# Kernel optimization log

Hardware: AMD Instinct MI355X
Metric: run time of the kernel (lower is better)

Reference implementation:

```python
import jax, jax.numpy as jnp
import numpy as np

B, T, D_F, L = 64, 256, 32, 128

def setup_inputs() -> dict:
    key = jax.random.key(0)
    k1, k2, k3, k4, k5 = jax.random.split(key, 5)
    return {
        "x": jax.random.normal(k1, (B, T, D_F), dtype=jnp.float32),
        "latent": jax.random.normal(k2, (B, T, L), dtype=jnp.float32),
        "kernel": jax.random.normal(k3, (1, 1, D_F, L), dtype=jnp.float32) * (6.0 / (D_F + L)) ** 0.5,
        "bias": jax.random.uniform(k4, (1, 1, D_F, L), dtype=jnp.float32),
        "unnorm_beta": jax.random.uniform(k5, (1, T, 1), dtype=jnp.float32),
    }

def reference(x, latent, kernel, bias, unnorm_beta):
    # features: [B,T,D_f,L]
    features = jax.nn.relu(x[..., None] * kernel + bias)
    # normal equations: X^T X over latent axis -> [B,T,D_f,D_f]
    xtx = jnp.einsum('btdl,btel->btde', features, features)
    xtx_inv = jnp.linalg.inv(xtx)
    # X^T y: [B,T,D_f]
    xty = jnp.einsum('btdl,btl->btd', features, latent)
    scores = jnp.einsum('btde,bte->btd', xtx_inv, xty)  # [B,T,D_f]
    # o_hat: weighted sum of feature rows -> [B,T,L]
    o_hat = jnp.einsum('btd,btdl->btl', scores, features)
    # L1-normalized attention over time: [1,T,1]
    abs_b = jnp.abs(unnorm_beta)
    weights = abs_b / jnp.sum(abs_b, axis=1)
    return jnp.sum(o_hat * weights, axis=1)  # [B,L]
```

## Files before the change

kernel.cpp:

```cpp
#include <hip/hip_runtime.h>
#include <stdint.h>

#define B_ 64
#define T_ 256
#define DF 32
#define L_ 128
#define AW 34
#define SLICE 4352

typedef float  v2f    __attribute__((ext_vector_type(2)));
typedef float  f32x16 __attribute__((ext_vector_type(16)));
typedef short  bf16x8 __attribute__((ext_vector_type(8)));

#define WAVE_SYNC() do { asm volatile("s_waitcnt lgkmcnt(0)" ::: "memory"); \
                         __builtin_amdgcn_sched_barrier(0); } while (0)

template <int IMM>
__device__ __forceinline__ float swz_f(float v) {
    return __builtin_bit_cast(float, __builtin_amdgcn_ds_swizzle(
        __builtin_bit_cast(int, v), IMM));
}
__device__ __forceinline__ uint32_t cvt_pk_bf16(float a, float b) {
    uint32_t r;
    asm("v_cvt_pk_bf16_f32 %0, %1, %2" : "=v"(r) : "v"(a), "v"(b));
    return r;
}
__device__ __forceinline__ float lo_f(uint32_t p) { return __builtin_bit_cast(float, p << 16); }
__device__ __forceinline__ float hi_f(uint32_t p) { return __builtin_bit_cast(float, p & 0xFFFF0000u); }

struct frag3 { bf16x8 h, m, l; };
union U8 { uint32_t u[4]; bf16x8 v; };

__device__ __forceinline__ frag3 split3(float4 a, float4 b) {
    uint32_t h0 = cvt_pk_bf16(a.x, a.y), h1 = cvt_pk_bf16(a.z, a.w);
    uint32_t h2 = cvt_pk_bf16(b.x, b.y), h3 = cvt_pk_bf16(b.z, b.w);
    float e0 = a.x - lo_f(h0), e1 = a.y - hi_f(h0);
    float e2 = a.z - lo_f(h1), e3 = a.w - hi_f(h1);
    float e4 = b.x - lo_f(h2), e5 = b.y - hi_f(h2);
    float e6 = b.z - lo_f(h3), e7 = b.w - hi_f(h3);
    uint32_t m0 = cvt_pk_bf16(e0, e1), m1 = cvt_pk_bf16(e2, e3);
    uint32_t m2 = cvt_pk_bf16(e4, e5), m3 = cvt_pk_bf16(e6, e7);
    float g0 = e0 - lo_f(m0), g1 = e1 - hi_f(m0);
    float g2 = e2 - lo_f(m1), g3 = e3 - hi_f(m1);
    float g4 = e4 - lo_f(m2), g5 = e5 - hi_f(m2);
    float g6 = e6 - lo_f(m3), g7 = e7 - hi_f(m3);
    uint32_t l0 = cvt_pk_bf16(g0, g1), l1 = cvt_pk_bf16(g2, g3);
    uint32_t l2 = cvt_pk_bf16(g4, g5), l3 = cvt_pk_bf16(g6, g7);
    U8 H, M, L;
    H.u[0] = h0; H.u[1] = h1; H.u[2] = h2; H.u[3] = h3;
    M.u[0] = m0; M.u[1] = m1; M.u[2] = m2; M.u[3] = m3;
    L.u[0] = l0; L.u[1] = l1; L.u[2] = l2; L.u[3] = l3;
    frag3 r; r.h = H.v; r.m = M.v; r.l = L.v; return r;
}

__device__ __forceinline__ f32x16 mfma32(bf16x8 a, bf16x8 b, f32x16 c) {
    return __builtin_amdgcn_mfma_f32_32x32x16_bf16(a, b, c, 0, 0, 0);
}

template <int K>
__device__ __forceinline__ void gj_round(float (&A)[33], float& dinv, int r) {
    float piv = swz_f<(K << 5)>(A[K]);
    float ip = __builtin_amdgcn_rcpf(piv);
    ip = ip * (2.0f - piv * ip);
    const bool isk = (r == K);
    float fmul = isk ? 0.f : A[K] * ip;
    dinv = isk ? ip : dinv;
    #pragma unroll
    for (int m = K + 1; m < 33; ++m) {
        float pk = swz_f<(K << 5)>(A[m]);
        A[m] = fmaf(-fmul, pk, A[m]);
    }
}

template <int K>
struct GJ {
    static __device__ __forceinline__ void run(float (&A)[33], float& dinv, int r) {
        gj_round<K>(A, dinv, r);
        GJ<K + 1>::run(A, dinv, r);
    }
};
template <>
struct GJ<32> {
    static __device__ __forceinline__ void run(float (&)[33], float&, int) {}
};

__global__ __launch_bounds__(64) void feat_kernel(
    const float* __restrict__ x,
    const float* __restrict__ latent,
    const float* __restrict__ kern,
    const float* __restrict__ bias,
    const float* __restrict__ beta,
    float* __restrict__ out,
    int mode)
{
    __shared__ __align__(16) char smem[2 * SLICE];
    const int lane = threadIdx.x;
    const int btA  = blockIdx.x * 2;
    const int btB  = btA + 1;

    const int g = lane >> 5;
    const int r = lane & 31;

    float* AsA = reinterpret_cast<float*>(smem);
    float* AsB = reinterpret_cast<float*>(smem + SLICE);

    const float4* kern4 = reinterpret_cast<const float4*>(kern);
    const float4* bias4 = reinterpret_cast<const float4*>(bias);
    const float4* latA4 = reinterpret_cast<const float4*>(latent) + (size_t)btA * 32;
    const float4* latB4 = reinterpret_cast<const float4*>(latent) + (size_t)btB * 32;

    const float xA = x[(size_t)btA * DF + r];
    const float xB = x[(size_t)btB * DF + r];

    f32x16 GA, GB;
    #pragma unroll
    for (int i = 0; i < 16; ++i) { GA[i] = 0.f; GB[i] = 0.f; }
    float ayA = 0.f, ayB = 0.f;

    #pragma unroll 2
    for (int ks = 0; ks < 8; ++ks) {
        const int idx = r * 32 + ks * 4 + g * 2;
        float4 Ka = kern4[idx],  Kb = kern4[idx + 1];
        float4 Ba = bias4[idx],  Bb = bias4[idx + 1];

        float4 faA, fbA, faB, fbB;
        faA.x = fmaxf(fmaf(xA, Ka.x, Ba.x), 0.f);
        faA.y = fmaxf(fmaf(xA, Ka.y, Ba.y), 0.f);
        faA.z = fmaxf(fmaf(xA, Ka.z, Ba.z), 0.f);
        faA.w = fmaxf(fmaf(xA, Ka.w, Ba.w), 0.f);
        fbA.x = fmaxf(fmaf(xA, Kb.x, Bb.x), 0.f);
        fbA.y = fmaxf(fmaf(xA, Kb.y, Bb.y), 0.f);
        fbA.z = fmaxf(fmaf(xA, Kb.z, Bb.z), 0.f);
        fbA.w = fmaxf(fmaf(xA, Kb.w, Bb.w), 0.f);
        faB.x = fmaxf(fmaf(xB, Ka.x, Ba.x), 0.f);
        faB.y = fmaxf(fmaf(xB, Ka.y, Ba.y), 0.f);
        faB.z = fmaxf(fmaf(xB, Ka.z, Ba.z), 0.f);
        faB.w = fmaxf(fmaf(xB, Ka.w, Ba.w), 0.f);
        fbB.x = fmaxf(fmaf(xB, Kb.x, Bb.x), 0.f);
        fbB.y = fmaxf(fmaf(xB, Kb.y, Bb.y), 0.f);
        fbB.z = fmaxf(fmaf(xB, Kb.z, Bb.z), 0.f);
        fbB.w = fmaxf(fmaf(xB, Kb.w, Bb.w), 0.f);

        float4 laA = latA4[ks * 4 + g * 2], lbA = latA4[ks * 4 + g * 2 + 1];
        float4 laB = latB4[ks * 4 + g * 2], lbB = latB4[ks * 4 + g * 2 + 1];
        ayA = fmaf(faA.x, laA.x, ayA); ayA = fmaf(faA.y, laA.y, ayA);
        ayA = fmaf(faA.z, laA.z, ayA); ayA = fmaf(faA.w, laA.w, ayA);
        ayA = fmaf(fbA.x, lbA.x, ayA); ayA = fmaf(fbA.y, lbA.y, ayA);
        ayA = fmaf(fbA.z, lbA.z, ayA); ayA = fmaf(fbA.w, lbA.w, ayA);
        ayB = fmaf(faB.x, laB.x, ayB); ayB = fmaf(faB.y, laB.y, ayB);
        ayB = fmaf(faB.z, laB.z, ayB); ayB = fmaf(faB.w, laB.w, ayB);
        ayB = fmaf(fbB.x, lbB.x, ayB); ayB = fmaf(fbB.y, lbB.y, ayB);
        ayB = fmaf(fbB.z, lbB.z, ayB); ayB = fmaf(fbB.w, lbB.w, ayB);

        frag3 FA = split3(faA, fbA);
        frag3 FB = split3(faB, fbB);
        GA = mfma32(FA.h, FA.h, GA);
        GB = mfma32(FB.h, FB.h, GB);
        GA = mfma32(FA.h, FA.m, GA);
        GB = mfma32(FB.h, FB.m, GB);
        GA = mfma32(FA.m, FA.h, GA);
        GB = mfma32(FB.m, FB.h, GB);
        GA = mfma32(FA.h, FA.l, GA);
        GB = mfma32(FB.h, FB.l, GB);
        GA = mfma32(FA.l, FA.h, GA);
        GB = mfma32(FB.l, FB.h, GB);
        GA = mfma32(FA.m, FA.m, GA);
        GB = mfma32(FB.m, FB.m, GB);
    }
    ayA += __shfl_xor(ayA, 32);
    ayB += __shfl_xor(ayB, 32);

    #pragma unroll
    for (int reg = 0; reg < 16; ++reg) {
        const int row = (reg & 3) + 8 * (reg >> 2) + 4 * g;
        AsA[row * AW + r] = GA[reg];
        AsB[row * AW + r] = GB[reg];
    }
    if (g == 0) AsA[r * AW + 32] = ayA;
    else        AsB[r * AW + 32] = ayB;
    WAVE_SYNC();

    float A[33];
    {
        const float* Amy = g ? AsB : AsA;
        #pragma unroll
        for (int m = 0; m < 16; ++m) {
            v2f t = *reinterpret_cast<const v2f*>(&Amy[r * AW + 2 * m]);
            A[2 * m]     = t[0];
            A[2 * m + 1] = t[1];
        }
        A[32] = Amy[r * AW + 32];
    }

    float dinv = 0.f;
    GJ<0>::run(A, dinv, r);
    const float s = A[32] * dinv;

    {
        float4 oA = make_float4(0.f, 0.f, 0.f, 0.f);
        float4 oB = make_float4(0.f, 0.f, 0.f, 0.f);
        #pragma unroll
        for (int dd = 0; dd < 16; ++dd) {
            int d = g * 16 + dd;
            float4 K  = kern4[d * 32 + r];
            float4 Bv = bias4[d * 32 + r];
            float xvA = __shfl(xA, d);
            float xvB = __shfl(xB, d);
            float sA  = __shfl(s, d);
            float sB  = __shfl(s, 32 + d);
            float fx = fmaxf(fmaf(xvA, K.x, Bv.x), 0.f);
            float fy = fmaxf(fmaf(xvA, K.y, Bv.y), 0.f);
            float fz = fmaxf(fmaf(xvA, K.z, Bv.z), 0.f);
            float fw = fmaxf(fmaf(xvA, K.w, Bv.w), 0.f);
            oA.x = fmaf(sA, fx, oA.x);
            oA.y = fmaf(sA, fy, oA.y);
            oA.z = fmaf(sA, fz, oA.z);
            oA.w = fmaf(sA, fw, oA.w);
            fx = fmaxf(fmaf(xvB, K.x, Bv.x), 0.f);
            fy = fmaxf(fmaf(xvB, K.y, Bv.y), 0.f);
            fz = fmaxf(fmaf(xvB, K.z, Bv.z), 0.f);
            fw = fmaxf(fmaf(xvB, K.w, Bv.w), 0.f);
            oB.x = fmaf(sB, fx, oB.x);
            oB.y = fmaf(sB, fy, oB.y);
            oB.z = fmaf(sB, fz, oB.z);
            oB.w = fmaf(sB, fw, oB.w);
        }
        oA.x += __shfl_xor(oA.x, 32); oA.y += __shfl_xor(oA.y, 32);
        oA.z += __shfl_xor(oA.z, 32); oA.w += __shfl_xor(oA.w, 32);
        oB.x += __shfl_xor(oB.x, 32); oB.y += __shfl_xor(oB.y, 32);
        oB.z += __shfl_xor(oB.z, 32); oB.w += __shfl_xor(oB.w, 32);

        if (mode == 0) {
            if (g == 0) reinterpret_cast<float4*>(out)[(size_t)btA * 32 + r] = oA;
            else        reinterpret_cast<float4*>(out)[(size_t)btB * 32 + r] = oB;
        } else {
            float v = fabsf(beta[lane]) + fabsf(beta[lane + 64]) +
                      fabsf(beta[lane + 128]) + fabsf(beta[lane + 192]);
            #pragma unroll
            for (int off = 32; off > 0; off >>= 1) v += __shfl_down(v, off);
            float S = __shfl(v, 0);
            const int tA = btA & (T_ - 1), tB = btB & (T_ - 1);
            const int b  = btA >> 8;
            if (g == 0) {
                float w_t = fabsf(beta[tA]) / S;
                float* op = &out[(size_t)b * L_ + 4 * r];
                atomicAdd(op + 0, oA.x * w_t);
                atomicAdd(op + 1, oA.y * w_t);
                atomicAdd(op + 2, oA.z * w_t);
                atomicAdd(op + 3, oA.w * w_t);
            } else {
                float w_t = fabsf(beta[tB]) / S;
                float* op = &out[(size_t)b * L_ + 4 * r];
                atomicAdd(op + 0, oB.x * w_t);
                atomicAdd(op + 1, oB.y * w_t);
                atomicAdd(op + 2, oB.z * w_t);
                atomicAdd(op + 3, oB.w * w_t);
            }
        }
    }
}

__global__ __launch_bounds__(256) void reduce_kernel(
    const float* __restrict__ ws,
    const float* __restrict__ beta,
    float* __restrict__ out)
{
    __shared__ float wsh[T_];
    __shared__ __align__(16) float4 par[8][32];
    __shared__ float red[4];
    const int b = blockIdx.x, tid = threadIdx.x;

    float bv = fabsf(beta[tid]);
    wsh[tid] = bv;
    float v = bv;
    #pragma unroll
    for (int o = 32; o > 0; o >>= 1) v += __shfl_down(v, o);
    if ((tid & 63) == 0) red[tid >> 6] = v;
    __syncthreads();
    const float S = red[0] + red[1] + red[2] + red[3];

    const int c = tid & 31, gg = tid >> 5;
    const float4* ws4 = reinterpret_cast<const float4*>(ws);
    float4 a = make_float4(0.f, 0.f, 0.f, 0.f);
    #pragma unroll 4
    for (int tt = 0; tt < 32; ++tt) {
        int t = gg * 32 + tt;
        float w = wsh[t];
        float4 u = ws4[((size_t)b * T_ + t) * 32 + c];
        a.x = fmaf(u.x, w, a.x);
        a.y = fmaf(u.y, w, a.y);
        a.z = fmaf(u.z, w, a.z);
        a.w = fmaf(u.w, w, a.w);
    }
    par[gg][c] = a;
    __syncthreads();
    if (tid < 32) {
        float4 s = par[0][tid];
        #pragma unroll
        for (int p = 1; p < 8; ++p) {
            float4 u = par[p][tid];
            s.x += u.x; s.y += u.y; s.z += u.z; s.w += u.w;
        }
        float inv = 1.0f / S;
        s.x *= inv; s.y *= inv; s.z *= inv; s.w *= inv;
        reinterpret_cast<float4*>(out)[b * 32 + tid] = s;
    }
}

extern "C" void kernel_launch(void* const* d_in, const int* in_sizes, int n_in,
                              void* d_out, int out_size, void* d_ws, size_t ws_size,
                              hipStream_t stream) {
    const float* x      = (const float*)d_in[0];
    const float* latent = (const float*)d_in[1];
    const float* kern   = (const float*)d_in[2];
    const float* bias   = (const float*)d_in[3];
    const float* beta   = (const float*)d_in[4];
    float* out = (float*)d_out;

    const size_t need = (size_t)B_ * T_ * L_ * sizeof(float);
    if (ws_size >= need) {
        float* ws = (float*)d_ws;
        feat_kernel<<<(B_ * T_) / 2, 64, 0, stream>>>(x, latent, kern, bias, beta, ws, 0);
        reduce_kernel<<<B_, 256, 0, stream>>>(ws, beta, out);
    } else {
        (void)hipMemsetAsync(d_out, 0, (size_t)out_size * sizeof(float), stream);
        feat_kernel<<<(B_ * T_) / 2, 64, 0, stream>>>(x, latent, kern, bias, beta, out, 1);
    }
}
```

Baseline: 72.20 us.

## Process four positions per block and interleave two Gauss-Jordan solves

```diff
diff --git a/kernel.cpp b/kernel.cpp
--- a/kernel.cpp
+++ b/kernel.cpp
@@ -57,61 +57,11 @@
     return __builtin_amdgcn_mfma_f32_32x32x16_bf16(a, b, c, 0, 0, 0);
 }
 
-template <int K>
-__device__ __forceinline__ void gj_round(float (&A)[33], float& dinv, int r) {
-    float piv = swz_f<(K << 5)>(A[K]);
-    float ip = __builtin_amdgcn_rcpf(piv);
-    ip = ip * (2.0f - piv * ip);
-    const bool isk = (r == K);
-    float fmul = isk ? 0.f : A[K] * ip;
-    dinv = isk ? ip : dinv;
-    #pragma unroll
-    for (int m = K + 1; m < 33; ++m) {
-        float pk = swz_f<(K << 5)>(A[m]);
-        A[m] = fmaf(-fmul, pk, A[m]);
-    }
-}
-
-template <int K>
-struct GJ {
-    static __device__ __forceinline__ void run(float (&A)[33], float& dinv, int r) {
-        gj_round<K>(A, dinv, r);
-        GJ<K + 1>::run(A, dinv, r);
-    }
-};
-template <>
-struct GJ<32> {
-    static __device__ __forceinline__ void run(float (&)[33], float&, int) {}
-};
-
-__global__ __launch_bounds__(64) void feat_kernel(
-    const float* __restrict__ x,
-    const float* __restrict__ latent,
-    const float* __restrict__ kern,
-    const float* __restrict__ bias,
-    const float* __restrict__ beta,
-    float* __restrict__ out,
-    int mode)
+__device__ __forceinline__ void gram_pair(
+    const float4* __restrict__ kern4, const float4* __restrict__ bias4,
+    const float4* __restrict__ latA4, const float4* __restrict__ latB4,
+    float xA, float xB, int r, int g, float* sA, float* sB)
 {
-    __shared__ __align__(16) char smem[2 * SLICE];
-    const int lane = threadIdx.x;
-    const int btA  = blockIdx.x * 2;
-    const int btB  = btA + 1;
-
-    const int g = lane >> 5;
-    const int r = lane & 31;
-
-    float* AsA = reinterpret_cast<float*>(smem);
-    float* AsB = reinterpret_cast<float*>(smem + SLICE);
-
-    const float4* kern4 = reinterpret_cast<const float4*>(kern);
-    const float4* bias4 = reinterpret_cast<const float4*>(bias);
-    const float4* latA4 = reinterpret_cast<const float4*>(latent) + (size_t)btA * 32;
-    const float4* latB4 = reinterpret_cast<const float4*>(latent) + (size_t)btB * 32;
-
-    const float xA = x[(size_t)btA * DF + r];
-    const float xB = x[(size_t)btB * DF + r];
-
     f32x16 GA, GB;
     #pragma unroll
     for (int i = 0; i < 16; ++i) { GA[i] = 0.f; GB[i] = 0.f; }
@@ -173,88 +123,183 @@
     #pragma unroll
     for (int reg = 0; reg < 16; ++reg) {
         const int row = (reg & 3) + 8 * (reg >> 2) + 4 * g;
-        AsA[row * AW + r] = GA[reg];
-        AsB[row * AW + r] = GB[reg];
-    }
-    if (g == 0) AsA[r * AW + 32] = ayA;
-    else        AsB[r * AW + 32] = ayB;
+        sA[row * AW + r] = GA[reg];
+        sB[row * AW + r] = GB[reg];
+    }
+    if (g == 0) sA[r * AW + 32] = ayA;
+    else        sB[r * AW + 32] = ayB;
+}
+
+template <int K>
+__device__ __forceinline__ void gj_round(float (&Aab)[33], float (&Acd)[33],
+                                         float& dab, float& dcd, int r) {
+    float pab = swz_f<(K << 5)>(Aab[K]);
+    float pcd = swz_f<(K << 5)>(Acd[K]);
+    float iab = __builtin_amdgcn_rcpf(pab);
+    float icd = __builtin_amdgcn_rcpf(pcd);
+    const bool isk = (r == K);
+    float fab = isk ? 0.f : Aab[K] * iab;
+    float fcd = isk ? 0.f : Acd[K] * icd;
+    dab = isk ? iab : dab;
+    dcd = isk ? icd : dcd;
+    #pragma unroll
+    for (int m = K + 1; m < 33; ++m) {
+        float kab = swz_f<(K << 5)>(Aab[m]);
+        float kcd = swz_f<(K << 5)>(Acd[m]);
+        Aab[m] = fmaf(-fab, kab, Aab[m]);
+        Acd[m] = fmaf(-fcd, kcd, Acd[m]);
+    }
+}
+
+template <int K>
+struct GJ {
+    static __device__ __forceinline__ void run(float (&Aab)[33], float (&Acd)[33],
+                                               float& dab, float& dcd, int r) {
+        gj_round<K>(Aab, Acd, dab, dcd, r);
+        GJ<K + 1>::run(Aab, Acd, dab, dcd, r);
+    }
+};
+template <>
+struct GJ<32> {
+    static __device__ __forceinline__ void run(float (&)[33], float (&)[33],
+                                               float&, float&, int) {}
+};
+
+__global__ __launch_bounds__(64) void feat_kernel(
+    const float* __restrict__ x,
+    const float* __restrict__ latent,
+    const float* __restrict__ kern,
+    const float* __restrict__ bias,
+    const float* __restrict__ beta,
+    float* __restrict__ out,
+    int mode)
+{
+    __shared__ __align__(16) char smem[4 * SLICE];
+    const int lane = threadIdx.x;
+    const int bt0  = blockIdx.x * 4;
+
+    const int g = lane >> 5;
+    const int r = lane & 31;
+
+    float* As0 = reinterpret_cast<float*>(smem);
+    float* As1 = reinterpret_cast<float*>(smem + SLICE);
+    float* As2 = reinterpret_cast<float*>(smem + 2 * SLICE);
+    float* As3 = reinterpret_cast<float*>(smem + 3 * SLICE);
+
+    const float4* kern4 = reinterpret_cast<const float4*>(kern);
+    const float4* bias4 = reinterpret_cast<const float4*>(bias);
+    const float4* lat4  = reinterpret_cast<const float4*>(latent);
+
+    const float xA = x[(size_t)(bt0 + 0) * DF + r];
+    const float xB = x[(size_t)(bt0 + 1) * DF + r];
+    const float xC = x[(size_t)(bt0 + 2) * DF + r];
+    const float xD = x[(size_t)(bt0 + 3) * DF + r];
+
+    gram_pair(kern4, bias4, lat4 + (size_t)(bt0 + 0) * 32, lat4 + (size_t)(bt0 + 1) * 32,
+              xA, xB, r, g, As0, As1);
+    gram_pair(kern4, bias4, lat4 + (size_t)(bt0 + 2) * 32, lat4 + (size_t)(bt0 + 3) * 32,
+              xC, xD, r, g, As2, As3);
     WAVE_SYNC();
 
-    float A[33];
+    float Aab[33], Acd[33];
     {
-        const float* Amy = g ? AsB : AsA;
+        const float* p1 = g ? As1 : As0;
+        const float* p2 = g ? As3 : As2;
         #pragma unroll
         for (int m = 0; m < 16; ++m) {
-            v2f t = *reinterpret_cast<const v2f*>(&Amy[r * AW + 2 * m]);
-            A[2 * m]     = t[0];
-            A[2 * m + 1] = t[1];
+            v2f t1 = *reinterpret_cast<const v2f*>(&p1[r * AW + 2 * m]);
+            v2f t2 = *reinterpret_cast<const v2f*>(&p2[r * AW + 2 * m]);
+            Aab[2 * m] = t1[0]; Aab[2 * m + 1] = t1[1];
+            Acd[2 * m] = t2[0]; Acd[2 * m + 1] = t2[1];
         }
-        A[32] = Amy[r * AW + 32];
-    }
-
-    float dinv = 0.f;
-    GJ<0>::run(A, dinv, r);
-    const float s = A[32] * dinv;
+        Aab[32] = p1[r * AW + 32];
+        Acd[32] = p2[r * AW + 32];
+    }
+
+    float dab = 0.f, dcd = 0.f;
+    GJ<0>::run(Aab, Acd, dab, dcd, r);
+    const float sab = Aab[32] * dab;
+    const float scd = Acd[32] * dcd;
 
     {
         float4 oA = make_float4(0.f, 0.f, 0.f, 0.f);
         float4 oB = make_float4(0.f, 0.f, 0.f, 0.f);
+        float4 oC = make_float4(0.f, 0.f, 0.f, 0.f);
+        float4 oD = make_float4(0.f, 0.f, 0.f, 0.f);
         #pragma unroll
         for (int dd = 0; dd < 16; ++dd) {
             int d = g * 16 + dd;
             float4 K  = kern4[d * 32 + r];
             float4 Bv = bias4[d * 32 + r];
-            float xvA = __shfl(xA, d);
-            float xvB = __shfl(xB, d);
-            float sA  = __shfl(s, d);
-            float sB  = __shfl(s, 32 + d);
-            float fx = fmaxf(fmaf(xvA, K.x, Bv.x), 0.f);
-            float fy = fmaxf(fmaf(xvA, K.y, Bv.y), 0.f);
-            float fz = fmaxf(fmaf(xvA, K.z, Bv.z), 0.f);
-            float fw = fmaxf(fmaf(xvA, K.w, Bv.w), 0.f);
-            oA.x = fmaf(sA, fx, oA.x);
-            oA.y = fmaf(sA, fy, oA.y);
-            oA.z = fmaf(sA, fz, oA.z);
-            oA.w = fmaf(sA, fw, oA.w);
+            float xvA = __shfl(xA, d), xvB = __shfl(xB, d);
+            float xvC = __shfl(xC, d), xvD = __shfl(xD, d);
+            float sA = __shfl(sab, d),      sB = __shfl(sab, 32 + d);
+            float sC = __shfl(scd, d),      sD = __shfl(scd, 32 + d);
+            float fx, fy, fz, fw;
+            fx = fmaxf(fmaf(xvA, K.x, Bv.x), 0.f);
+            fy = fmaxf(fmaf(xvA, K.y, Bv.y), 0.f);
+            fz = fmaxf(fmaf(xvA, K.z, Bv.z), 0.f);
+            fw = fmaxf(fmaf(xvA, K.w, Bv.w), 0.f);
+            oA.x = fmaf(sA, fx, oA.x); oA.y = fmaf(sA, fy, oA.y);
+            oA.z = fmaf(sA, fz, oA.z); oA.w = fmaf(sA, fw, oA.w);
             fx = fmaxf(fmaf(xvB, K.x, Bv.x), 0.f);
             fy = fmaxf(fmaf(xvB, K.y, Bv.y), 0.f);
             fz = fmaxf(fmaf(xvB, K.z, Bv.z), 0.f);
             fw = fmaxf(fmaf(xvB, K.w, Bv.w), 0.f);
-            oB.x = fmaf(sB, fx, oB.x);
-            oB.y = fmaf(sB, fy, oB.y);
-            oB.z = fmaf(sB, fz, oB.z);
-            oB.w = fmaf(sB, fw, oB.w);
+            oB.x = fmaf(sB, fx, oB.x); oB.y = fmaf(sB, fy, oB.y);
+            oB.z = fmaf(sB, fz, oB.z); oB.w = fmaf(sB, fw, oB.w);
+            fx = fmaxf(fmaf(xvC, K.x, Bv.x), 0.f);
+            fy = fmaxf(fmaf(xvC, K.y, Bv.y), 0.f);
+            fz = fmaxf(fmaf(xvC, K.z, Bv.z), 0.f);
+            fw = fmaxf(fmaf(xvC, K.w, Bv.w), 0.f);
+            oC.x = fmaf(sC, fx, oC.x); oC.y = fmaf(sC, fy, oC.y);
+            oC.z = fmaf(sC, fz, oC.z); oC.w = fmaf(sC, fw, oC.w);
+            fx = fmaxf(fmaf(xvD, K.x, Bv.x), 0.f);
+            fy = fmaxf(fmaf(xvD, K.y, Bv.y), 0.f);
+            fz = fmaxf(fmaf(xvD, K.z, Bv.z), 0.f);
+            fw = fmaxf(fmaf(xvD, K.w, Bv.w), 0.f);
+            oD.x = fmaf(sD, fx, oD.x); oD.y = fmaf(sD, fy, oD.y);
+            oD.z = fmaf(sD, fz, oD.z); oD.w = fmaf(sD, fw, oD.w);
         }
         oA.x += __shfl_xor(oA.x, 32); oA.y += __shfl_xor(oA.y, 32);
         oA.z += __shfl_xor(oA.z, 32); oA.w += __shfl_xor(oA.w, 32);
         oB.x += __shfl_xor(oB.x, 32); oB.y += __shfl_xor(oB.y, 32);
         oB.z += __shfl_xor(oB.z, 32); oB.w += __shfl_xor(oB.w, 32);
+        oC.x += __shfl_xor(oC.x, 32); oC.y += __shfl_xor(oC.y, 32);
+        oC.z += __shfl_xor(oC.z, 32); oC.w += __shfl_xor(oC.w, 32);
+        oD.x += __shfl_xor(oD.x, 32); oD.y += __shfl_xor(oD.y, 32);
+        oD.z += __shfl_xor(oD.z, 32); oD.w += __shfl_xor(oD.w, 32);
 
         if (mode == 0) {
-            if (g == 0) reinterpret_cast<float4*>(out)[(size_t)btA * 32 + r] = oA;
-            else        reinterpret_cast<float4*>(out)[(size_t)btB * 32 + r] = oB;
+            if (g == 0) {
+                reinterpret_cast<float4*>(out)[(size_t)(bt0 + 0) * 32 + r] = oA;
+                reinterpret_cast<float4*>(out)[(size_t)(bt0 + 2) * 32 + r] = oC;
+            } else {
+                reinterpret_cast<float4*>(out)[(size_t)(bt0 + 1) * 32 + r] = oB;
+                reinterpret_cast<float4*>(out)[(size_t)(bt0 + 3) * 32 + r] = oD;
+            }
         } else {
             float v = fabsf(beta[lane]) + fabsf(beta[lane + 64]) +
                       fabsf(beta[lane + 128]) + fabsf(beta[lane + 192]);
             #pragma unroll
             for (int off = 32; off > 0; off >>= 1) v += __shfl_down(v, off);
             float S = __shfl(v, 0);
-            const int tA = btA & (T_ - 1), tB = btB & (T_ - 1);
-            const int b  = btA >> 8;
+            const int b = bt0 >> 8;
+            float* op = &out[(size_t)b * L_ + 4 * r];
             if (g == 0) {
-                float w_t = fabsf(beta[tA]) / S;
-                float* op = &out[(size_t)b * L_ + 4 * r];
-                atomicAdd(op + 0, oA.x * w_t);
-                atomicAdd(op + 1, oA.y * w_t);
-                atomicAdd(op + 2, oA.z * w_t);
-                atomicAdd(op + 3, oA.w * w_t);
+                float wA = fabsf(beta[(bt0 + 0) & (T_ - 1)]) / S;
+                float wC = fabsf(beta[(bt0 + 2) & (T_ - 1)]) / S;
+                atomicAdd(op + 0, oA.x * wA + oC.x * wC);
+                atomicAdd(op + 1, oA.y * wA + oC.y * wC);
+                atomicAdd(op + 2, oA.z * wA + oC.z * wC);
+                atomicAdd(op + 3, oA.w * wA + oC.w * wC);
             } else {
-                float w_t = fabsf(beta[tB]) / S;
-                float* op = &out[(size_t)b * L_ + 4 * r];
-                atomicAdd(op + 0, oB.x * w_t);
-                atomicAdd(op + 1, oB.y * w_t);
-                atomicAdd(op + 2, oB.z * w_t);
-                atomicAdd(op + 3, oB.w * w_t);
+                float wB = fabsf(beta[(bt0 + 1) & (T_ - 1)]) / S;
+                float wD = fabsf(beta[(bt0 + 3) & (T_ - 1)]) / S;
+                atomicAdd(op + 0, oB.x * wB + oD.x * wD);
+                atomicAdd(op + 1, oB.y * wB + oD.y * wD);
+                atomicAdd(op + 2, oB.z * wB + oD.z * wD);
+                atomicAdd(op + 3, oB.w * wB + oD.w * wD);
             }
         }
     }
@@ -320,10 +365,10 @@
     const size_t need = (size_t)B_ * T_ * L_ * sizeof(float);
     if (ws_size >= need) {
         float* ws = (float*)d_ws;
-        feat_kernel<<<(B_ * T_) / 2, 64, 0, stream>>>(x, latent, kern, bias, beta, ws, 0);
+        feat_kernel<<<(B_ * T_) / 4, 64, 0, stream>>>(x, latent, kern, bias, beta, ws, 0);
         reduce_kernel<<<B_, 256, 0, stream>>>(ws, beta, out);
     } else {
         (void)hipMemsetAsync(d_out, 0, (size_t)out_size * sizeof(float), stream);
-        feat_kernel<<<(B_ * T_) / 2, 64, 0, stream>>>(x, latent, kern, bias, beta, out, 1);
-    }
-}
+        feat_kernel<<<(B_ * T_) / 4, 64, 0, stream>>>(x, latent, kern, bias, beta, out, 1);
+    }
+}
```

After: 78.84 us. 9.2% more time.
